# Kernel tuning notes

Measured on AMD Instinct MI355X. Metric: run time of the kernel, lower is better.

Reference implementation:

```python
import jax, jax.numpy as jnp
import numpy as np

NUM_HEADS = 16
NUM_UNITS = 1024
NEG = -2.0**32 + 1.0
EPS = 1e-8


def setup_inputs() -> dict:
    key = jax.random.key(0)
    ks = jax.random.split(key, 8)
    B, T, C = 2, 2048, 1024
    U = NUM_UNITS
    x = jax.random.normal(ks[0], (B, T, C), dtype=jnp.float32)
    s = 1.0 / np.sqrt(C)
    Wq = jax.random.normal(ks[1], (C, U), dtype=jnp.float32) * s
    Wk = jax.random.normal(ks[2], (C, U), dtype=jnp.float32) * s
    Wv = jax.random.normal(ks[3], (C, U), dtype=jnp.float32) * s
    bq = jnp.zeros((U,), dtype=jnp.float32)
    bk = jnp.zeros((U,), dtype=jnp.float32)
    bv = jnp.zeros((U,), dtype=jnp.float32)
    gamma = jnp.ones((U,), dtype=jnp.float32)
    beta = jnp.zeros((U,), dtype=jnp.float32)
    return {"x": x, "Wq": Wq, "bq": bq, "Wk": Wk, "bk": bk,
            "Wv": Wv, "bv": bv, "gamma": gamma, "beta": beta}


def _attention(x, Wq, bq, Wk, bk, Wv, bv, gamma, beta):
    B, T, C = x.shape
    H = NUM_HEADS
    U = NUM_UNITS
    dh = U // H
    # Dense projections with relu activation (Keras Dense(activation='relu'))
    Q = jax.nn.relu(x @ Wq + bq)  # [B, T, U]
    K = jax.nn.relu(x @ Wk + bk)
    V = jax.nn.relu(x @ Wv + bv)
    # split into heads: tf.split(axis=2) + concat(axis=0) == [B, T, H, dh]
    Qh = Q.reshape(B, T, H, dh)
    Kh = K.reshape(B, T, H, dh)
    Vh = V.reshape(B, T, H, dh)
    # scaled dot-product scores: scale by sqrt(d_head) (K_ last dim after split)
    scores = jnp.einsum('bqhd,bkhd->bhqk', Qh, Kh) / np.sqrt(dh)
    # key mask: sign(|sum(keys, -1)|) over the ORIGINAL keys input (= x)
    key_mask = jnp.sign(jnp.abs(jnp.sum(x, axis=-1)))  # [B, Tk]
    scores = jnp.where(key_mask[:, None, None, :] == 0, NEG, scores)
    # causal mask (lower-triangular)
    tril = jnp.tril(jnp.ones((T, T), dtype=scores.dtype))
    scores = jnp.where(tril[None, None, :, :] == 0, NEG, scores)
    attn = jax.nn.softmax(scores, axis=-1)
    # query mask: multiply attention rows for zero queries
    query_mask = jnp.sign(jnp.abs(jnp.sum(x, axis=-1)))  # [B, Tq]
    attn = attn * query_mask[:, None, :, None]
    # dropout rate is 0 -> identity
    out = jnp.einsum('bhqk,bkhd->bqhd', attn, Vh).reshape(B, T, U)
    # residual with original queries
    out = out + x
    # layer norm over last axis (tf.nn.moments: biased variance)
    mean = jnp.mean(out, axis=-1, keepdims=True)
    var = jnp.mean((out - mean) ** 2, axis=-1, keepdims=True)
    normalized = (out - mean) / jnp.sqrt(var + EPS)
    return gamma * normalized + beta


def reference(x, Wq, bq, Wk, bk, Wv, bv, gamma, beta):
    return _attention(x, Wq, bq, Wk, bk, Wv, bv, gamma, beta)
```

## Files before the change

kernel.cpp:

```cpp
#include <hip/hip_runtime.h>
#include <math.h>

#define BB 2
#define TT 2048
#define CC 1024
#define UU 1024
#define HH 16
#define DH 64
#define BT (BB*TT)

typedef __attribute__((ext_vector_type(8))) __bf16 bf16x8;
typedef __attribute__((ext_vector_type(4))) __bf16 bf16x4;
typedef __attribute__((ext_vector_type(4))) float f32x4;

#define GLL16(g, l) __builtin_amdgcn_global_load_lds( \
    (__attribute__((address_space(1))) const void*)(g), \
    (__attribute__((address_space(3))) void*)(l), 16, 0, 0)

#define C2EXP 0.18033688011112042f
#define MBIAS 64.0f

__global__ __launch_bounds__(256) void prep_kernel(
    const float* __restrict__ x, float* __restrict__ kadd, __bf16* __restrict__ xb,
    const float* __restrict__ Wq, const float* __restrict__ Wk,
    const float* __restrict__ Wv, __bf16* __restrict__ Wt) {
    const int bx = blockIdx.x;
    const int t = threadIdx.x;
    if (bx < BT) {
        int row = bx;
        float4 v = *(const float4*)&x[(size_t)row * CC + t * 4];
        bf16x4 o;
        o[0] = (__bf16)v.x; o[1] = (__bf16)v.y; o[2] = (__bf16)v.z; o[3] = (__bf16)v.w;
        *(bf16x4*)&xb[(size_t)row * CC + t * 4] = o;
        float s = v.x + v.y + v.z + v.w;
#pragma unroll
        for (int off = 32; off; off >>= 1) s += __shfl_down(s, off, 64);
        __shared__ float red[4];
        int lane = t & 63, w = t >> 6;
        if (lane == 0) red[w] = s;
        __syncthreads();
        if (t == 0) {
            float tot = red[0] + red[1] + red[2] + red[3];
            kadd[row] = (tot == 0.f ? -1.0e30f : 0.f) - MBIAS;
        }
    } else {
        int bz = bx - BT;
        int z = bz >> 8, rem = bz & 255;
        const float* W = z == 0 ? Wq : (z == 1 ? Wk : Wv);
        __bf16* Out = Wt + (size_t)z * CC * UU;
        __shared__ float tile[64][65];
        int n0 = (rem & 15) * 64, k0 = (rem >> 4) * 64;
        int r = t >> 4, c4 = (t & 15) * 4;
#pragma unroll
        for (int i = 0; i < 4; ++i) {
            float4 v = *(const float4*)&W[(size_t)(k0 + r + i * 16) * UU + n0 + c4];
            tile[r + i * 16][c4 + 0] = v.x; tile[r + i * 16][c4 + 1] = v.y;
            tile[r + i * 16][c4 + 2] = v.z; tile[r + i * 16][c4 + 3] = v.w;
        }
        __syncthreads();
#pragma unroll
        for (int i = 0; i < 4; ++i) {
            int nr = r + i * 16;
            bf16x4 o;
            o[0] = (__bf16)tile[c4 + 0][nr]; o[1] = (__bf16)tile[c4 + 1][nr];
            o[2] = (__bf16)tile[c4 + 2][nr]; o[3] = (__bf16)tile[c4 + 3][nr];
            *(bf16x4*)&Out[(size_t)(n0 + nr) * CC + k0 + c4] = o;
        }
    }
}

__global__ __launch_bounds__(256, 4) void qkv_mfma(
    const __bf16* __restrict__ xb, const __bf16* __restrict__ Wt_all,
    const float* __restrict__ bq, const float* __restrict__ bk,
    const float* __restrict__ bv,
    __bf16* __restrict__ Qo, __bf16* __restrict__ Ko, __bf16* __restrict__ VTo) {
    const int z = blockIdx.z;
    const __bf16* Wt = Wt_all + (size_t)z * CC * UU;
    const float* bias = z == 0 ? bq : (z == 1 ? bk : bv);

    const int n0 = blockIdx.x * 128, m0 = blockIdx.y * 128;
    const int t = threadIdx.x, w = t >> 6, lane = t & 63;
    const int quad = lane >> 4, nn = lane & 15;
    const int wr = w >> 1, wc = w & 1;

    __shared__ __bf16 smem[2 * 128 * 64];
    __bf16* As = smem;
    __bf16* Bs = smem + 128 * 64;

    f32x4 acc[4][4];
#pragma unroll
    for (int i = 0; i < 4; ++i)
#pragma unroll
        for (int j = 0; j < 4; ++j) acc[i][j] = (f32x4){0.f, 0.f, 0.f, 0.f};

    for (int k0 = 0; k0 < CC; k0 += 64) {
        __syncthreads();
#pragma unroll
        for (int i = 0; i < 4; ++i) {
            int c = i * 256 + t;
            int row = c >> 3;
            int gc = ((c & 7) ^ (row & 7)) * 8;
            GLL16(&xb[(size_t)(m0 + row) * CC + k0 + gc], &As[c * 8]);
            GLL16(&Wt[(size_t)(n0 + row) * CC + k0 + gc], &Bs[c * 8]);
        }
        __syncthreads();
#pragma unroll
        for (int kk = 0; kk < 2; ++kk) {
            bf16x8 af[4], bfr[4];
#pragma unroll
            for (int i = 0; i < 4; ++i) {
                int R = wr * 64 + i * 16 + nn;
                af[i] = *(const bf16x8*)&As[R * 64 + (((kk * 4 + quad) ^ (R & 7)) * 8)];
            }
#pragma unroll
            for (int j = 0; j < 4; ++j) {
                int R = wc * 64 + j * 16 + nn;
                bfr[j] = *(const bf16x8*)&Bs[R * 64 + (((kk * 4 + quad) ^ (R & 7)) * 8)];
            }
#pragma unroll
            for (int i = 0; i < 4; ++i)
#pragma unroll
                for (int j = 0; j < 4; ++j)
                    acc[i][j] = __builtin_amdgcn_mfma_f32_16x16x32_bf16(af[i], bfr[j], acc[i][j], 0, 0, 0);
        }
    }

    __bf16* cw = &smem[w * 1024];
    float bv4[4];
#pragma unroll
    for (int j = 0; j < 4; ++j) bv4[j] = bias[n0 + wc * 64 + j * 16 + nn];

    if (z < 2) {
        __bf16* Out = z == 0 ? Qo : Ko;
#pragma unroll
        for (int i = 0; i < 4; ++i) {
            __syncthreads();
#pragma unroll
            for (int j = 0; j < 4; ++j)
#pragma unroll
                for (int r = 0; r < 4; ++r)
                    cw[(quad * 4 + r) * 64 + j * 16 + nn] =
                        (__bf16)fmaxf(acc[i][j][r] + bv4[j], 0.f);
            __syncthreads();
            int rr = lane >> 2, cc = (lane & 3) * 16;
            bf16x8 v0 = *(const bf16x8*)&cw[rr * 64 + cc];
            bf16x8 v1 = *(const bf16x8*)&cw[rr * 64 + cc + 8];
            size_t o = (size_t)(m0 + wr * 64 + i * 16 + rr) * UU + n0 + wc * 64 + cc;
            *(bf16x8*)&Out[o] = v0;
            *(bf16x8*)&Out[o + 8] = v1;
        }
    } else {
#pragma unroll
        for (int i = 0; i < 4; ++i) {
            __syncthreads();
#pragma unroll
            for (int j = 0; j < 4; ++j)
#pragma unroll
                for (int r = 0; r < 4; ++r)
                    cw[(j * 16 + nn) * 16 + quad * 4 + r] =
                        (__bf16)fmaxf(acc[i][j][r] + bv4[j], 0.f);
            __syncthreads();
            bf16x8 v0 = *(const bf16x8*)&cw[lane * 16];
            bf16x8 v1 = *(const bf16x8*)&cw[lane * 16 + 8];
            size_t o = (size_t)(n0 + wc * 64 + lane) * BT + m0 + wr * 64 + i * 16;
            *(bf16x8*)&VTo[o] = v0;
            *(bf16x8*)&VTo[o + 8] = v1;
        }
    }
}

__global__ __launch_bounds__(256, 3) void attn_mfma(
    const __bf16* __restrict__ Q, const __bf16* __restrict__ K,
    const __bf16* __restrict__ Vt, const float* __restrict__ kadd,
    __bf16* __restrict__ Ob) {
    const int bx = blockIdx.x;
    const int bh = blockIdx.y, b = bh >> 4, h = bh & 15;
    const int j = bh >> 3;
    const int xj = (j & 2) ? ((bx + 16) & 31) : bx;
    const int qt = (j & 1) ? (31 - xj) : xj;
    const int col0 = h * 64, rowbase = b * TT, q0 = qt * 64;

    const int t = threadIdx.x;
    const int w = t >> 6, lane = t & 63, quad = lane >> 4, nn = lane & 15;
    const int s7 = nn & 7;

    __shared__ __align__(16) __bf16 ks[3][64 * 64];
    __shared__ __align__(16) __bf16 vt[2][64 * 64];
    __shared__ __align__(16) __bf16 ps[64 * 64];

    const int c0 = t;
    const int r0 = c0 >> 3, g0 = ((c0 & 7) ^ (r0 & 7)) * 8;
    const int prow = 16 * w + nn;
    const int qg = q0 + prow;

    const __bf16* kp0 = &K[(size_t)(rowbase + r0) * UU + col0 + g0];
    const __bf16* kp1 = kp0 + 32 * (size_t)UU;
    const __bf16* vp0 = &Vt[(size_t)(col0 + r0) * BT + rowbase + g0];
    const __bf16* vp1 = vp0 + 32 * (size_t)BT;
    const float* kap = &kadd[rowbase + quad * 4];

    f32x4 ka[4];
#pragma unroll
    for (int ct = 0; ct < 4; ++ct) ka[ct] = *(const f32x4*)&kap[ct * 16];
    kap += 64;
    const __bf16* qrow = &Q[(size_t)(rowbase + qg) * UU + col0];
    bf16x8 bq0 = *(const bf16x8*)&qrow[quad * 8];
    bf16x8 bq1 = *(const bf16x8*)&qrow[32 + quad * 8];
    __builtin_amdgcn_sched_barrier(0);
    GLL16(kp0, &ks[0][c0 * 8]);
    GLL16(kp1, &ks[0][c0 * 8 + 2048]);
    GLL16(vp0, &vt[0][c0 * 8]);
    GLL16(vp1, &vt[0][c0 * 8 + 2048]);
    kp0 += 64 * (size_t)UU; kp1 += 64 * (size_t)UU;
    vp0 += 64; vp1 += 64;
    __builtin_amdgcn_sched_barrier(0);
    GLL16(kp0, &ks[0][4096 + c0 * 8]);
    GLL16(kp1, &ks[0][4096 + c0 * 8 + 2048]);
    kp0 += 64 * (size_t)UU; kp1 += 64 * (size_t)UU;
    __builtin_amdgcn_sched_barrier(0);
    asm volatile("s_waitcnt vmcnt(2)" ::: "memory");
    __builtin_amdgcn_s_barrier();

    float lp = 0.f;
    f32x4 oc[4];
#pragma unroll
    for (int dt = 0; dt < 4; ++dt) oc[dt] = (f32x4){0.f, 0.f, 0.f, 0.f};

#define ATTN_CORE(KOFF, VOFF, DIAG)                                            \
  {                                                                            \
    const __bf16* ksc = &ks[0][0] + (KOFF);                                    \
    const __bf16* vtc = &vt[0][0] + (VOFF);                                    \
    _Pragma("unroll")                                                          \
    for (int ct = 0; ct < 4; ++ct) {                                           \
      int krow = ct * 16 + nn;                                                 \
      bf16x8 a0 = *(const bf16x8*)&ksc[krow * 64 + ((quad ^ s7) * 8)];         \
      bf16x8 a1 = *(const bf16x8*)&ksc[krow * 64 + (((4 + quad) ^ s7) * 8)];   \
      f32x4 sc = (f32x4){0.f, 0.f, 0.f, 0.f};                                  \
      sc = __builtin_amdgcn_mfma_f32_16x16x32_bf16(a0, bq0, sc, 0, 0, 0);      \
      sc = __builtin_amdgcn_mfma_f32_16x16x32_bf16(a1, bq1, sc, 0, 0, 0);      \
      bf16x4 pw;                                                               \
      _Pragma("unroll")                                                        \
      for (int r = 0; r < 4; ++r) {                                            \
        float arg = fmaf(sc[r], C2EXP, ka[ct][r]);                             \
        if (DIAG) {                                                            \
          int kl = ct * 16 + quad * 4 + r;                                     \
          if (kl > prow) arg = -1.0e30f;                                       \
        }                                                                      \
        float p = __builtin_amdgcn_exp2f(arg);                                 \
        lp += p;                                                               \
        pw[r] = (__bf16)p;                                                     \
      }                                                                        \
      int chunk = ct * 2 + (quad >> 1);                                        \
      *(bf16x4*)&ps[prow * 64 + ((chunk ^ s7) * 8) + (quad & 1) * 4] = pw;     \
    }                                                                          \
    bf16x8 bp0 = *(const bf16x8*)&ps[prow * 64 + ((quad ^ s7) * 8)];           \
    bf16x8 bp1 = *(const bf16x8*)&ps[prow * 64 + (((4 + quad) ^ s7) * 8)];     \
    _Pragma("unroll")                                                          \
    for (int dt = 0; dt < 4; ++dt) {                                           \
      int vrow = dt * 16 + nn;                                                 \
      bf16x8 a0 = *(const bf16x8*)&vtc[vrow * 64 + ((quad ^ s7) * 8)];         \
      bf16x8 a1 = *(const bf16x8*)&vtc[vrow * 64 + (((4 + quad) ^ s7) * 8)];   \
      oc[dt] = __builtin_amdgcn_mfma_f32_16x16x32_bf16(a0, bp0, oc[dt], 0, 0, 0); \
      oc[dt] = __builtin_amdgcn_mfma_f32_16x16x32_bf16(a1, bp1, oc[dt], 0, 0, 0); \
    }                                                                          \
  }

    int kro = 0, kwo = 2 * 4096, vo = 0;
    for (int kt = 0; kt < qt; ++kt) {
        f32x4 kan[4];
#pragma unroll
        for (int ct = 0; ct < 4; ++ct) kan[ct] = *(const f32x4*)&kap[ct * 16];
        kap += 64;
        __builtin_amdgcn_sched_barrier(0);
        GLL16(vp0, &vt[0][(vo ^ 4096) + c0 * 8]);
        GLL16(vp1, &vt[0][(vo ^ 4096) + c0 * 8 + 2048]);
        vp0 += 64; vp1 += 64;
        __builtin_amdgcn_sched_barrier(0);
        GLL16(kp0, &ks[0][kwo + c0 * 8]);
        GLL16(kp1, &ks[0][kwo + c0 * 8 + 2048]);
        kp0 += 64 * (size_t)UU; kp1 += 64 * (size_t)UU;
        __builtin_amdgcn_sched_barrier(0);
        ATTN_CORE(kro, vo, false)
#pragma unroll
        for (int ct = 0; ct < 4; ++ct) ka[ct] = kan[ct];
        kro = kro == 8192 ? 0 : kro + 4096;
        kwo = kwo == 8192 ? 0 : kwo + 4096;
        vo ^= 4096;
        asm volatile("s_waitcnt vmcnt(2)" ::: "memory");
        __builtin_amdgcn_s_barrier();
    }
    ATTN_CORE(kro, vo, true)
#undef ATTN_CORE

    float l = lp;
    l += __shfl_xor(l, 16, 64);
    l += __shfl_xor(l, 32, 64);
    int grow = rowbase + qg;
    float qsel = (kadd[grow] < -1.0e29f) ? 0.f : 1.f;
    float mult = qsel / fmaxf(l, 1e-37f);
#pragma unroll
    for (int dt = 0; dt < 4; ++dt) {
        bf16x4 ov;
        ov[0] = (__bf16)(oc[dt][0] * mult); ov[1] = (__bf16)(oc[dt][1] * mult);
        ov[2] = (__bf16)(oc[dt][2] * mult); ov[3] = (__bf16)(oc[dt][3] * mult);
        *(bf16x4*)&Ob[(size_t)grow * UU + col0 + dt * 16 + quad * 4] = ov;
    }
}

__global__ __launch_bounds__(256) void ln_kernel(
    const __bf16* __restrict__ Ob, const float* __restrict__ x,
    const float* __restrict__ gamma, const float* __restrict__ beta,
    float* __restrict__ out) {
    int row = blockIdx.x;
    size_t base = (size_t)row * UU;
    int t = threadIdx.x;
    bf16x4 ov = *(const bf16x4*)&Ob[base + t * 4];
    float4 xv = *(const float4*)&x[base + t * 4];
    float v0 = (float)ov[0] + xv.x, v1 = (float)ov[1] + xv.y;
    float v2 = (float)ov[2] + xv.z, v3 = (float)ov[3] + xv.w;
    float s1 = v0 + v1 + v2 + v3;
    float s2 = v0 * v0 + v1 * v1 + v2 * v2 + v3 * v3;
#pragma unroll
    for (int off = 32; off; off >>= 1) {
        s1 += __shfl_down(s1, off, 64);
        s2 += __shfl_down(s2, off, 64);
    }
    __shared__ float r1[4], r2[4];
    int lane = t & 63, w = t >> 6;
    if (lane == 0) { r1[w] = s1; r2[w] = s2; }
    __syncthreads();
    s1 = r1[0] + r1[1] + r1[2] + r1[3];
    s2 = r2[0] + r2[1] + r2[2] + r2[3];
    float mean = s1 * (1.0f / 1024.0f);
    float var = s2 * (1.0f / 1024.0f) - mean * mean;
    float rstd = rsqrtf(var + 1e-8f);
    float4 g = *(const float4*)&gamma[t * 4];
    float4 be = *(const float4*)&beta[t * 4];
    float4 ores;
    ores.x = g.x * (v0 - mean) * rstd + be.x;
    ores.y = g.y * (v1 - mean) * rstd + be.y;
    ores.z = g.z * (v2 - mean) * rstd + be.z;
    ores.w = g.w * (v3 - mean) * rstd + be.w;
    *(float4*)&out[base + t * 4] = ores;
}

extern "C" void kernel_launch(void* const* d_in, const int* in_sizes, int n_in,
                              void* d_out, int out_size, void* d_ws, size_t ws_size,
                              hipStream_t stream) {
    const float* x     = (const float*)d_in[0];
    const float* Wq    = (const float*)d_in[1];
    const float* bq    = (const float*)d_in[2];
    const float* Wk    = (const float*)d_in[3];
    const float* bk    = (const float*)d_in[4];
    const float* Wv    = (const float*)d_in[5];
    const float* bv    = (const float*)d_in[6];
    const float* gamma = (const float*)d_in[7];
    const float* beta  = (const float*)d_in[8];
    float* out = (float*)d_out;

    char* wsb = (char*)d_ws;
    const size_t MB = 1024ull * 1024;
    __bf16* xb = (__bf16*)(wsb);
    __bf16* Wt = (__bf16*)(wsb + 8 * MB);
    __bf16* Ob = (__bf16*)(wsb);
    __bf16* Qb = (__bf16*)(wsb + 16 * MB);
    __bf16* Kb = (__bf16*)(wsb + 24 * MB);
    __bf16* Vt = (__bf16*)(wsb + 32 * MB);
    float* kadd = (float*)(wsb + 40 * MB);

    prep_kernel<<<dim3(BT + 768), dim3(256), 0, stream>>>(x, kadd, xb, Wq, Wk, Wv, Wt);
    qkv_mfma<<<dim3(UU / 128, BT / 128, 3), dim3(256), 0, stream>>>(
        xb, Wt, bq, bk, bv, Qb, Kb, Vt);
    attn_mfma<<<dim3(32, BB * HH), dim3(256), 0, stream>>>(Qb, Kb, Vt, kadd, Ob);
    ln_kernel<<<dim3(BT), dim3(256), 0, stream>>>(Ob, x, gamma, beta, out);
}
```

Measured before the change: 171.1 us.

## Split long causal query tiles across two key-range blocks and merge in layernorm

Query tiles in the second half of the sequence now have their key range split between two blocks. Each block writes unnormalized fp32 partial outputs and row sums, and the layernorm kernel adds the partials and applies the softmax normalization and query mask. The aim is to shorten the longest causal block and improve load balance across 48 blocks per head. In exchange, the key buffer drops from triple to double buffering with a full vmcnt(0) wait each iteration, occupancy is raised to 4, and there is extra fp32 partial-output traffic to global memory.

Result: slower. 180.6 us (+5.5%).

```diff
diff --git a/kernel.cpp b/kernel.cpp
--- a/kernel.cpp
+++ b/kernel.cpp
@@ -169,22 +169,31 @@
     }
 }
 
-__global__ __launch_bounds__(256, 3) void attn_mfma(
+__global__ __launch_bounds__(256, 4) void attn_mfma(
     const __bf16* __restrict__ Q, const __bf16* __restrict__ K,
     const __bf16* __restrict__ Vt, const float* __restrict__ kadd,
-    __bf16* __restrict__ Ob) {
-    const int bx = blockIdx.x;
+    float* __restrict__ Op0, float* __restrict__ Op1,
+    float* __restrict__ lq0, float* __restrict__ lq1) {
+    const int cx = blockIdx.x;
     const int bh = blockIdx.y, b = bh >> 4, h = bh & 15;
-    const int j = bh >> 3;
-    const int xj = (j & 2) ? ((bx + 16) & 31) : bx;
-    const int qt = (j & 1) ? (31 - xj) : xj;
+    int qt, kst, ket, slot;
+    if (cx < 16) { qt = cx; kst = 0; ket = qt; slot = 0; }
+    else {
+        int q2 = (cx - 16) >> 1;
+        qt = 16 + q2;
+        int len0 = (qt + 2) >> 1;
+        slot = (cx - 16) & 1;
+        if (slot) { kst = len0; ket = qt; }
+        else      { kst = 0;    ket = len0 - 1; }
+    }
     const int col0 = h * 64, rowbase = b * TT, q0 = qt * 64;
+    const bool hasdiag = (ket == qt);
 
     const int t = threadIdx.x;
     const int w = t >> 6, lane = t & 63, quad = lane >> 4, nn = lane & 15;
     const int s7 = nn & 7;
 
-    __shared__ __align__(16) __bf16 ks[3][64 * 64];
+    __shared__ __align__(16) __bf16 ks[2][64 * 64];
     __shared__ __align__(16) __bf16 vt[2][64 * 64];
     __shared__ __align__(16) __bf16 ps[64 * 64];
 
@@ -193,11 +202,11 @@
     const int prow = 16 * w + nn;
     const int qg = q0 + prow;
 
-    const __bf16* kp0 = &K[(size_t)(rowbase + r0) * UU + col0 + g0];
+    const __bf16* kp0 = &K[(size_t)(rowbase + kst * 64 + r0) * UU + col0 + g0];
     const __bf16* kp1 = kp0 + 32 * (size_t)UU;
-    const __bf16* vp0 = &Vt[(size_t)(col0 + r0) * BT + rowbase + g0];
+    const __bf16* vp0 = &Vt[(size_t)(col0 + r0) * BT + rowbase + kst * 64 + g0];
     const __bf16* vp1 = vp0 + 32 * (size_t)BT;
-    const float* kap = &kadd[rowbase + quad * 4];
+    const float* kap = &kadd[rowbase + kst * 64 + quad * 4];
 
     f32x4 ka[4];
 #pragma unroll
@@ -206,19 +215,14 @@
     const __bf16* qrow = &Q[(size_t)(rowbase + qg) * UU + col0];
     bf16x8 bq0 = *(const bf16x8*)&qrow[quad * 8];
     bf16x8 bq1 = *(const bf16x8*)&qrow[32 + quad * 8];
-    __builtin_amdgcn_sched_barrier(0);
+
     GLL16(kp0, &ks[0][c0 * 8]);
     GLL16(kp1, &ks[0][c0 * 8 + 2048]);
     GLL16(vp0, &vt[0][c0 * 8]);
     GLL16(vp1, &vt[0][c0 * 8 + 2048]);
     kp0 += 64 * (size_t)UU; kp1 += 64 * (size_t)UU;
     vp0 += 64; vp1 += 64;
-    __builtin_amdgcn_sched_barrier(0);
-    GLL16(kp0, &ks[0][4096 + c0 * 8]);
-    GLL16(kp1, &ks[0][4096 + c0 * 8 + 2048]);
-    kp0 += 64 * (size_t)UU; kp1 += 64 * (size_t)UU;
-    __builtin_amdgcn_sched_barrier(0);
-    asm volatile("s_waitcnt vmcnt(2)" ::: "memory");
+    asm volatile("s_waitcnt vmcnt(0)" ::: "memory");
     __builtin_amdgcn_s_barrier();
 
     float lp = 0.f;
@@ -226,10 +230,10 @@
 #pragma unroll
     for (int dt = 0; dt < 4; ++dt) oc[dt] = (f32x4){0.f, 0.f, 0.f, 0.f};
 
-#define ATTN_CORE(KOFF, VOFF, DIAG)                                            \
+#define ATTN_CORE(KSC, VTC, DIAG)                                              \
   {                                                                            \
-    const __bf16* ksc = &ks[0][0] + (KOFF);                                    \
-    const __bf16* vtc = &vt[0][0] + (VOFF);                                    \
+    const __bf16* ksc = (KSC);                                                 \
+    const __bf16* vtc = (VTC);                                                 \
     _Pragma("unroll")                                                          \
     for (int ct = 0; ct < 4; ++ct) {                                           \
       int krow = ct * 16 + nn;                                                 \
@@ -265,59 +269,71 @@
     }                                                                          \
   }
 
-    int kro = 0, kwo = 2 * 4096, vo = 0;
-    for (int kt = 0; kt < qt; ++kt) {
+    int cur = 0;
+    for (int kt = kst; kt < ket; ++kt) {
         f32x4 kan[4];
 #pragma unroll
         for (int ct = 0; ct < 4; ++ct) kan[ct] = *(const f32x4*)&kap[ct * 16];
         kap += 64;
-        __builtin_amdgcn_sched_barrier(0);
-        GLL16(vp0, &vt[0][(vo ^ 4096) + c0 * 8]);
-        GLL16(vp1, &vt[0][(vo ^ 4096) + c0 * 8 + 2048]);
+        GLL16(kp0, &ks[cur ^ 1][c0 * 8]);
+        GLL16(kp1, &ks[cur ^ 1][c0 * 8 + 2048]);
+        GLL16(vp0, &vt[cur ^ 1][c0 * 8]);
+        GLL16(vp1, &vt[cur ^ 1][c0 * 8 + 2048]);
+        kp0 += 64 * (size_t)UU; kp1 += 64 * (size_t)UU;
         vp0 += 64; vp1 += 64;
-        __builtin_amdgcn_sched_barrier(0);
-        GLL16(kp0, &ks[0][kwo + c0 * 8]);
-        GLL16(kp1, &ks[0][kwo + c0 * 8 + 2048]);
-        kp0 += 64 * (size_t)UU; kp1 += 64 * (size_t)UU;
-        __builtin_amdgcn_sched_barrier(0);
-        ATTN_CORE(kro, vo, false)
+        ATTN_CORE(ks[cur], vt[cur], false)
 #pragma unroll
         for (int ct = 0; ct < 4; ++ct) ka[ct] = kan[ct];
-        kro = kro == 8192 ? 0 : kro + 4096;
-        kwo = kwo == 8192 ? 0 : kwo + 4096;
-        vo ^= 4096;
-        asm volatile("s_waitcnt vmcnt(2)" ::: "memory");
+        cur ^= 1;
+        asm volatile("s_waitcnt vmcnt(0)" ::: "memory");
         __builtin_amdgcn_s_barrier();
     }
-    ATTN_CORE(kro, vo, true)
+    if (hasdiag) {
+        ATTN_CORE(ks[cur], vt[cur], true)
+    } else {
+        ATTN_CORE(ks[cur], vt[cur], false)
+    }
 #undef ATTN_CORE
 
     float l = lp;
     l += __shfl_xor(l, 16, 64);
     l += __shfl_xor(l, 32, 64);
-    int grow = rowbase + qg;
-    float qsel = (kadd[grow] < -1.0e29f) ? 0.f : 1.f;
-    float mult = qsel / fmaxf(l, 1e-37f);
-#pragma unroll
-    for (int dt = 0; dt < 4; ++dt) {
-        bf16x4 ov;
-        ov[0] = (__bf16)(oc[dt][0] * mult); ov[1] = (__bf16)(oc[dt][1] * mult);
-        ov[2] = (__bf16)(oc[dt][2] * mult); ov[3] = (__bf16)(oc[dt][3] * mult);
-        *(bf16x4*)&Ob[(size_t)grow * UU + col0 + dt * 16 + quad * 4] = ov;
-    }
+    const int grow = rowbase + qg;
+    float* Op;
+    size_t orow;
+    if (slot) { Op = Op1; orow = (size_t)(grow - (b + 1) * 1024); }
+    else      { Op = Op0; orow = (size_t)grow; }
+    if (quad == 0) (slot ? lq1 : lq0)[(size_t)grow * HH + h] = l;
+#pragma unroll
+    for (int dt = 0; dt < 4; ++dt)
+        *(f32x4*)&Op[orow * UU + col0 + dt * 16 + quad * 4] = oc[dt];
 }
 
 __global__ __launch_bounds__(256) void ln_kernel(
-    const __bf16* __restrict__ Ob, const float* __restrict__ x,
+    const float* __restrict__ Op0, const float* __restrict__ Op1,
+    const float* __restrict__ lq0, const float* __restrict__ lq1,
+    const float* __restrict__ kadd, const float* __restrict__ x,
     const float* __restrict__ gamma, const float* __restrict__ beta,
     float* __restrict__ out) {
     int row = blockIdx.x;
+    int b = row >> 11;
+    int qt = (row & (TT - 1)) >> 6;
     size_t base = (size_t)row * UU;
     int t = threadIdx.x;
-    bf16x4 ov = *(const bf16x4*)&Ob[base + t * 4];
+    int h = t >> 4;
+    float l = lq0[(size_t)row * HH + h];
+    f32x4 o = *(const f32x4*)&Op0[base + t * 4];
+    if (qt >= 16) {
+        l += lq1[(size_t)row * HH + h];
+        size_t base1 = (size_t)(row - (b + 1) * 1024) * UU;
+        f32x4 o1 = *(const f32x4*)&Op1[base1 + t * 4];
+        o[0] += o1[0]; o[1] += o1[1]; o[2] += o1[2]; o[3] += o1[3];
+    }
+    float qsel = (kadd[row] < -1.0e29f) ? 0.f : 1.f;
+    float mult = qsel / fmaxf(l, 1e-37f);
     float4 xv = *(const float4*)&x[base + t * 4];
-    float v0 = (float)ov[0] + xv.x, v1 = (float)ov[1] + xv.y;
-    float v2 = (float)ov[2] + xv.z, v3 = (float)ov[3] + xv.w;
+    float v0 = o[0] * mult + xv.x, v1 = o[1] * mult + xv.y;
+    float v2 = o[2] * mult + xv.z, v3 = o[3] * mult + xv.w;
     float s1 = v0 + v1 + v2 + v3;
     float s2 = v0 * v0 + v1 * v1 + v2 * v2 + v3 * v3;
 #pragma unroll
@@ -362,15 +378,20 @@
     const size_t MB = 1024ull * 1024;
     __bf16* xb = (__bf16*)(wsb);
     __bf16* Wt = (__bf16*)(wsb + 8 * MB);
-    __bf16* Ob = (__bf16*)(wsb);
+    float* Op0 = (float*)(wsb);
     __bf16* Qb = (__bf16*)(wsb + 16 * MB);
     __bf16* Kb = (__bf16*)(wsb + 24 * MB);
     __bf16* Vt = (__bf16*)(wsb + 32 * MB);
     float* kadd = (float*)(wsb + 40 * MB);
+    float* Op1  = (float*)(wsb + 41 * MB);
+    float* lq0  = (float*)(wsb + 49 * MB);
+    float* lq1  = (float*)(wsb + 50 * MB);
 
     prep_kernel<<<dim3(BT + 768), dim3(256), 0, stream>>>(x, kadd, xb, Wq, Wk, Wv, Wt);
     qkv_mfma<<<dim3(UU / 128, BT / 128, 3), dim3(256), 0, stream>>>(
         xb, Wt, bq, bk, bv, Qb, Kb, Vt);
-    attn_mfma<<<dim3(32, BB * HH), dim3(256), 0, stream>>>(Qb, Kb, Vt, kadd, Ob);
-    ln_kernel<<<dim3(BT), dim3(256), 0, stream>>>(Ob, x, gamma, beta, out);
-}
+    attn_mfma<<<dim3(48, BB * HH), dim3(256), 0, stream>>>(
+        Qb, Kb, Vt, kadd, Op0, Op1, lq0, lq1);
+    ln_kernel<<<dim3(BT), dim3(256), 0, stream>>>(
+        Op0, Op1, lq0, lq1, kadd, x, gamma, beta, out);
+}
```
